# Kernel optimization log

Hardware: AMD Instinct MI355X
Metric: run time of the kernel (lower is better)

The kernel has to match this reference:

```python
import jax, jax.numpy as jnp
import numpy as np

B, L, D = 4, 2048, 512
H, DK, DV = 8, 64, 64


def setup_inputs() -> dict:
    key = jax.random.key(0)
    ks = jax.random.split(key, 12)
    s = 0.02
    return {
        "query": jax.random.normal(ks[0], (B, L, D), jnp.float32),
        "key": jax.random.normal(ks[1], (B, L, D), jnp.float32),
        "value": jax.random.normal(ks[2], (B, L, D), jnp.float32),
        "attention_mask": jax.random.normal(ks[3], (1, 1, L, L), jnp.float32),
        "Wq": jax.random.normal(ks[4], (D, H * DK), jnp.float32) * s,
        "bq": jnp.zeros((H * DK,), jnp.float32),
        "Wk": jax.random.normal(ks[5], (D, H * DK), jnp.float32) * s,
        "bk": jnp.zeros((H * DK,), jnp.float32),
        "Wv": jax.random.normal(ks[6], (D, H * DV), jnp.float32) * s,
        "bv": jnp.zeros((H * DV,), jnp.float32),
        "Wo": jax.random.normal(ks[7], (H * DV, D), jnp.float32) * s,
        "bo": jnp.zeros((D,), jnp.float32),
    }


def reference(query, key, value, attention_mask, Wq, bq, Wk, bk, Wv, bv, Wo, bo):
    sz_b, len_q, _ = query.shape
    len_k = key.shape[1]
    # projections -> [B, L, H, d]
    q = (query @ Wq + bq).reshape(sz_b, len_q, H, DK)
    k = (key @ Wk + bk).reshape(sz_b, len_k, H, DK)
    v = (value @ Wv + bv).reshape(sz_b, len_k, H, DV)
    # permute(2,0,1,3): heads first -> [H, B, L, d]
    q = jnp.transpose(q, (2, 0, 1, 3))
    k = jnp.transpose(k, (2, 0, 1, 3))
    v = jnp.transpose(v, (2, 0, 1, 3))
    scale = 1.0 / jnp.sqrt(jnp.asarray(DK, q.dtype))
    scores = jnp.einsum('hbqd,hbkd->hbqk', q, k) * scale + attention_mask
    attn = jax.nn.softmax(scores, axis=-1)
    x = jnp.einsum('hbqk,hbkd->hbqd', attn, v)  # [H, B, Lq, Dv]
    # faithful to torch: transpose(1,2) -> [H, Lq, B, Dv] then view(B, Lq, H*Dv)
    x = jnp.transpose(x, (0, 2, 1, 3)).reshape(sz_b, len_q, H * DV)
    return x @ Wo + bo
```

## Files before the change

kernel.cpp:

```cpp
#include <hip/hip_runtime.h>

#define SEQ    2048
#define DMODEL 512
#define NHEAD  8
#define HDIM   64
#define BATCH  4
#define NROWS  65536
#define KSPLIT 2

#define LOG2E  1.4426950408889634f
#define QSCALE 0.18033688011112042f

typedef float f32x4  __attribute__((ext_vector_type(4)));
typedef float f32x16 __attribute__((ext_vector_type(16)));
typedef _Float16 h16x8 __attribute__((ext_vector_type(8)));
typedef _Float16 h16x2 __attribute__((ext_vector_type(2)));
typedef unsigned int u32x2 __attribute__((ext_vector_type(2)));

union U4H { uint4 u; h16x8 h; };
union U1H2 { unsigned int u; h16x2 h; };

#define WAITV(N) asm volatile("s_waitcnt vmcnt(" #N ")" ::: "memory")

static __device__ inline h16x2 pkrtz(float a, float b) {
    return __builtin_bit_cast(h16x2, __builtin_amdgcn_cvt_pkrtz(a, b));
}
static __device__ inline unsigned short f2h(float x) {
    _Float16 h = (_Float16)x;
    return __builtin_bit_cast(unsigned short, h);
}
static __device__ inline void async_cp16(const void* g, void* l) {
    __builtin_amdgcn_global_load_lds(
        (const __attribute__((address_space(1))) unsigned int*)g,
        (__attribute__((address_space(3))) unsigned int*)l,
        16, 0, 0);
}

struct PrepArgs {
    const float *Wq, *Wk, *Wv, *Wo;
    unsigned short *WqT, *WkT, *WvT, *WoT;
    const float *mask; unsigned short *mp;
    const float *aq, *ak, *av;
    unsigned short *dq, *dk, *dv;
};

__global__ __launch_bounds__(256) void prepass(PrepArgs a) {
    const int bid = blockIdx.x;
    const int t = threadIdx.x;

    if (bid < 1024) {
        const int z = bid >> 8, y = (bid >> 4) & 15, x = bid & 15;
        const float* S; unsigned short* D;
        switch (z) {
            case 0: S = a.Wq; D = a.WqT; break;
            case 1: S = a.Wk; D = a.WkT; break;
            case 2: S = a.Wv; D = a.WvT; break;
            default: S = a.Wo; D = a.WoT; break;
        }
        __shared__ float T[32][33];
        const int r = t >> 3, c = (t & 7) * 4;
        const int k0 = x * 32, n0 = y * 32;
        float4 v = *(const float4*)&S[(size_t)(k0 + r) * DMODEL + n0 + c];
        T[r][c] = v.x; T[r][c + 1] = v.y; T[r][c + 2] = v.z; T[r][c + 3] = v.w;
        __syncthreads();
        ushort4 o;
        o.x = f2h(T[c + 0][r]); o.y = f2h(T[c + 1][r]);
        o.z = f2h(T[c + 2][r]); o.w = f2h(T[c + 3][r]);
        *(ushort4*)&D[(size_t)(n0 + r) * DMODEL + k0 + c] = o;
    } else if (bid < 1024 + 4096) {
        int i = (bid - 1024) * 256 + t;
        int k = (i * 4) & (SEQ - 1);
        int q = (i * 4) >> 11;
        float4 v = ((const float4*)a.mask)[i];
        int kt = k >> 6, kl = k & 63;
        int mt = kl >> 5, g = (kl >> 3) & 3, hl = (kl >> 2) & 1;
        size_t base = ((size_t)kt * SEQ + q) * 64 + hl * 32 + mt * 16 + g * 4;
        ushort4 o;
        o.x = f2h(__builtin_amdgcn_exp2f(v.x * LOG2E));
        o.y = f2h(__builtin_amdgcn_exp2f(v.y * LOG2E));
        o.z = f2h(__builtin_amdgcn_exp2f(v.z * LOG2E));
        o.w = f2h(__builtin_amdgcn_exp2f(v.w * LOG2E));
        *(ushort4*)&a.mp[base] = o;
    } else {
        int u = bid - 5120;
        int z = u >> 11, blk = u & 2047;
        const float* S; unsigned short* D;
        switch (z) {
            case 0: S = a.aq; D = a.dq; break;
            case 1: S = a.ak; D = a.dk; break;
            default: S = a.av; D = a.dv; break;
        }
        size_t i = ((size_t)blk * 256 + t) * 8;
        float4 x = *(const float4*)&S[i];
        float4 y = *(const float4*)&S[i + 4];
        U1H2 p0, p1, p2, p3;
        p0.h = pkrtz(x.x, x.y); p1.h = pkrtz(x.z, x.w);
        p2.h = pkrtz(y.x, y.y); p3.h = pkrtz(y.z, y.w);
        *(uint4*)&D[i] = make_uint4(p0.u, p1.u, p2.u, p3.u);
    }
}

template <int EPI>
static __device__ inline void gemm_core16(
    const unsigned short* __restrict__ Ab, const unsigned short* __restrict__ Bt,
    const float* __restrict__ bias, void* __restrict__ Cout, float oscale,
    int bm, int bn)
{
    __shared__ __align__(16) unsigned short As[3][128 * 32];
    __shared__ __align__(16) unsigned short Bs[3][128 * 32];

    const int t = threadIdx.x;
    const int lane = t & 63, w = t >> 6;
    const int wm = w >> 1, wn = w & 1;
    const int c = lane & 15, quad = lane >> 4;
    const int srow = lane >> 2;
    const int sck  = (lane & 3) ^ ((lane >> 3) & 3);

    f32x4 acc[4][4] = {};

    const int NT = DMODEL / 32;

    #pragma unroll
    for (int b2 = 0; b2 < 2; b2++) {
        #pragma unroll
        for (int i = 0; i < 2; i++) {
            int row = 32 * w + 16 * i + srow;
            async_cp16(Ab + (size_t)(bm + row) * DMODEL + b2 * 32 + sck * 8,
                       &As[b2][(32 * w + 16 * i) * 32]);
            async_cp16(Bt + (size_t)(bn + row) * DMODEL + b2 * 32 + sck * 8,
                       &Bs[b2][(32 * w + 16 * i) * 32]);
        }
    }
    WAITV(4);
    __builtin_amdgcn_s_barrier();

    const int slot8 = (quad ^ ((c >> 1) & 3)) * 8;

    int cur = 0;
    for (int p = 0; p < NT; p++) {
        if (p + 2 < NT) {
            int nxt = cur + 2; if (nxt >= 3) nxt -= 3;
            int kn = (p + 2) * 32;
            #pragma unroll
            for (int i = 0; i < 2; i++) {
                int row = 32 * w + 16 * i + srow;
                async_cp16(Ab + (size_t)(bm + row) * DMODEL + kn + sck * 8,
                           &As[nxt][(32 * w + 16 * i) * 32]);
                async_cp16(Bt + (size_t)(bn + row) * DMODEL + kn + sck * 8,
                           &Bs[nxt][(32 * w + 16 * i) * 32]);
            }
        }
        U4H af[4], bf[4];
        #pragma unroll
        for (int mt = 0; mt < 4; mt++)
            af[mt].u = *(const uint4*)&As[cur][(wm * 64 + mt * 16 + c) * 32 + slot8];
        #pragma unroll
        for (int nt = 0; nt < 4; nt++)
            bf[nt].u = *(const uint4*)&Bs[cur][(wn * 64 + nt * 16 + c) * 32 + slot8];
        #pragma unroll
        for (int mt = 0; mt < 4; mt++)
            #pragma unroll
            for (int nt = 0; nt < 4; nt++)
                acc[mt][nt] = __builtin_amdgcn_mfma_f32_16x16x32_f16(
                    af[mt].h, bf[nt].h, acc[mt][nt], 0, 0, 0);
        if (p + 1 < NT) {
            if (p + 2 < NT) { WAITV(4); } else { WAITV(0); }
            __builtin_amdgcn_s_barrier();
        }
        cur = cur + 1; if (cur >= 3) cur -= 3;
    }

    if (EPI == 2) {
        #pragma unroll
        for (int nt = 0; nt < 4; nt++) {
            int ng = bn + wn * 64 + nt * 16 + c;
            int h = ng >> 6, dv = ng & 63;
            float bv = bias[ng];
            #pragma unroll
            for (int mt = 0; mt < 4; mt++) {
                int mg0 = bm + wm * 64 + mt * 16 + quad * 4;
                int bb = mg0 >> 11, key0 = mg0 & (SEQ - 1);
                U1H2 lo, hi;
                lo.h = pkrtz(acc[mt][nt][0] + bv, acc[mt][nt][1] + bv);
                hi.h = pkrtz(acc[mt][nt][2] + bv, acc[mt][nt][3] + bv);
                *(uint2*)&((unsigned short*)Cout)[
                    ((size_t)(bb * NHEAD + h) * HDIM + dv) * SEQ + key0] =
                    make_uint2(lo.u, hi.u);
            }
        }
        return;
    }
    #pragma unroll
    for (int nt = 0; nt < 4; nt++) {
        int ng = bn + wn * 64 + nt * 16 + c;
        float bv = bias[ng];
        #pragma unroll
        for (int mt = 0; mt < 4; mt++) {
            #pragma unroll
            for (int r = 0; r < 4; r++) {
                int mg = bm + wm * 64 + mt * 16 + quad * 4 + r;
                float v = (acc[mt][nt][r] + bv) * oscale;
                if (EPI == 1)
                    ((unsigned short*)Cout)[(size_t)mg * DMODEL + ng] = f2h(v);
                else
                    ((float*)Cout)[(size_t)mg * DMODEL + ng] = v;
            }
        }
    }
}

struct QKVArgs {
    const unsigned short *A0, *A1, *A2;
    const unsigned short *W0, *W1, *W2;
    const float *b0, *b1, *b2;
    unsigned short *o0, *o1, *o2;
};

__global__ __launch_bounds__(256) void gemm_qkv(QKVArgs a) {
    if (blockIdx.z == 2)
        gemm_core16<2>(a.A2, a.W2, a.b2, a.o2, 1.0f, blockIdx.y * 128, blockIdx.x * 128);
    else if (blockIdx.z == 1)
        gemm_core16<1>(a.A1, a.W1, a.b1, a.o1, 1.0f, blockIdx.y * 128, blockIdx.x * 128);
    else
        gemm_core16<1>(a.A0, a.W0, a.b0, a.o0, QSCALE, blockIdx.y * 128, blockIdx.x * 128);
}

__global__ __launch_bounds__(256) void gemm_fin(
    const unsigned short* __restrict__ A, const unsigned short* __restrict__ W,
    const float* __restrict__ bias, float* __restrict__ C) {
    gemm_core16<0>(A, W, bias, C, 1.0f, blockIdx.y * 128, blockIdx.x * 128);
}

__global__ __launch_bounds__(256, 3) void attn5(
    const unsigned short* __restrict__ qb, const unsigned short* __restrict__ kb,
    const unsigned short* __restrict__ vT, const unsigned short* __restrict__ emp,
    unsigned short* __restrict__ Xp, float* __restrict__ Lp)
{
    __shared__ __align__(16) unsigned short Ks[3][64 * 64];
    __shared__ __align__(16) unsigned short Vs[3][64 * 64];

    const int t = threadIdx.x;
    const int lane = t & 63, w = t >> 6;
    const int c32 = lane & 31, hl = lane >> 5;
    const int bh = blockIdx.x, b = bh >> 3, head = bh & 7;
    const int q0 = blockIdx.y * 128;
    const int split = blockIdx.z;
    const int qg = q0 + w * 32 + c32;
    const int NT = 1024 / 64;

    const unsigned short* qrow = qb + ((size_t)b * SEQ + qg) * DMODEL + head * HDIM;
    U4H Qf[4];
    #pragma unroll
    for (int s = 0; s < 4; s++)
        Qf[s].u = *(const uint4*)&qrow[s * 16 + hl * 8];

    const unsigned short* kgb = kb + (size_t)b * SEQ * DMODEL + head * HDIM
                              + (size_t)split * 1024 * DMODEL;
    const unsigned short* vgb = vT + (size_t)bh * HDIM * SEQ + split * 1024;

    const int srow = lane >> 3;
    const int sch  = (lane & 7) ^ srow;

    U4H e0, e1, e2, e3;
    {
        const unsigned short* mrow = emp + ((size_t)(split * 16) * SEQ + qg) * 64 + hl * 32;
        e0.u = *(const uint4*)&mrow[0];
        e1.u = *(const uint4*)&mrow[8];
        e2.u = *(const uint4*)&mrow[16];
        e3.u = *(const uint4*)&mrow[24];
    }

    #pragma unroll
    for (int b2 = 0; b2 < 2; b2++) {
        int kq = b2 * 64;
        #pragma unroll
        for (int i = 0; i < 2; i++) {
            int row = w * 16 + i * 8 + srow;
            async_cp16(&kgb[(size_t)(kq + row) * DMODEL + sch * 8],
                       &Ks[b2][(w * 16 + i * 8) * 64]);
            async_cp16(&vgb[(size_t)row * SEQ + kq + sch * 8],
                       &Vs[b2][(w * 16 + i * 8) * 64]);
        }
    }
    WAITV(4);
    __builtin_amdgcn_s_barrier();

    f32x16 O0 = {}, O1 = {};
    float lsum = 0.f;
    const h16x2 one2 = {(_Float16)1.0f, (_Float16)1.0f};

    int cur = 0;
    for (int kt = 0; kt < NT; kt++) {
        U4H f0, f1, f2, f3;
        if (kt + 1 < NT) {
            const unsigned short* mrow =
                emp + ((size_t)(split * 16 + kt + 1) * SEQ + qg) * 64 + hl * 32;
            f0.u = *(const uint4*)&mrow[0];
            f1.u = *(const uint4*)&mrow[8];
            f2.u = *(const uint4*)&mrow[16];
            f3.u = *(const uint4*)&mrow[24];
        }

        if (kt + 2 < NT) {
            int nxt = cur + 2; if (nxt >= 3) nxt -= 3;
            int k0n = (kt + 2) * 64;
            #pragma unroll
            for (int i = 0; i < 2; i++) {
                int row = w * 16 + i * 8 + srow;
                async_cp16(&kgb[(size_t)(k0n + row) * DMODEL + sch * 8],
                           &Ks[nxt][(w * 16 + i * 8) * 64]);
                async_cp16(&vgb[(size_t)row * SEQ + k0n + sch * 8],
                           &Vs[nxt][(w * 16 + i * 8) * 64]);
            }
        }

        const unsigned short* Kp = Ks[cur];
        const unsigned short* Vp = Vs[cur];

        f32x16 S0 = {}, S1 = {};
        __builtin_amdgcn_s_setprio(1);
        #pragma unroll
        for (int s = 0; s < 4; s++) {
            int fc = 2 * s + hl;
            int sl = (fc ^ (c32 & 7)) * 8;
            U4H ka0, ka1;
            ka0.u = *(const uint4*)&Kp[c32 * 64 + sl];
            ka1.u = *(const uint4*)&Kp[(32 + c32) * 64 + sl];
            S0 = __builtin_amdgcn_mfma_f32_32x32x16_f16(ka0.h, Qf[s].h, S0, 0, 0, 0);
            S1 = __builtin_amdgcn_mfma_f32_32x32x16_f16(ka1.h, Qf[s].h, S1, 0, 0, 0);
        }
        __builtin_amdgcn_s_setprio(0);

        unsigned int Pf[4][4];
        #pragma unroll
        for (int mt = 0; mt < 2; mt++) {
            f32x16 S = mt ? S1 : S0;
            h16x8 ea = (mt ? e2 : e0).h;
            h16x8 eb = (mt ? e3 : e1).h;
            unsigned int u[4][2];
            #pragma unroll
            for (int jj = 0; jj < 8; jj++) {
                _Float16 exl = (jj < 4) ? ea[2 * jj]     : eb[2 * jj - 8];
                _Float16 exh = (jj < 4) ? ea[2 * jj + 1] : eb[2 * jj - 7];
                h16x2 ex = {exl, exh};
                h16x2 pk = pkrtz(__builtin_amdgcn_exp2f(S[2 * jj]),
                                 __builtin_amdgcn_exp2f(S[2 * jj + 1]));
                h16x2 pp = pk * ex;
#if __has_builtin(__builtin_amdgcn_fdot2)
                lsum = __builtin_amdgcn_fdot2(pp, one2, lsum, false);
#else
                lsum += (float)pp[0] + (float)pp[1];
#endif
                u[jj >> 1][jj & 1] = __builtin_bit_cast(unsigned int, pp);
            }
#if __has_builtin(__builtin_amdgcn_permlane32_swap)
            u32x2 rA0 = __builtin_amdgcn_permlane32_swap(u[0][0], u[1][0], false, false);
            u32x2 rA1 = __builtin_amdgcn_permlane32_swap(u[0][1], u[1][1], false, false);
            u32x2 rB0 = __builtin_amdgcn_permlane32_swap(u[2][0], u[3][0], false, false);
            u32x2 rB1 = __builtin_amdgcn_permlane32_swap(u[2][1], u[3][1], false, false);
            Pf[2 * mt + 0][0] = rA0[0]; Pf[2 * mt + 0][1] = rA1[0];
            Pf[2 * mt + 0][2] = rA0[1]; Pf[2 * mt + 0][3] = rA1[1];
            Pf[2 * mt + 1][0] = rB0[0]; Pf[2 * mt + 1][1] = rB1[0];
            Pf[2 * mt + 1][2] = rB0[1]; Pf[2 * mt + 1][3] = rB1[1];
#else
            unsigned int sA0 = hl ? u[0][0] : u[1][0];
            unsigned int sA1 = hl ? u[0][1] : u[1][1];
            unsigned int sB0 = hl ? u[2][0] : u[3][0];
            unsigned int sB1 = hl ? u[2][1] : u[3][1];
            unsigned int rA0 = (unsigned)__shfl_xor((int)sA0, 32, 64);
            unsigned int rA1 = (unsigned)__shfl_xor((int)sA1, 32, 64);
            unsigned int rB0 = (unsigned)__shfl_xor((int)sB0, 32, 64);
            unsigned int rB1 = (unsigned)__shfl_xor((int)sB1, 32, 64);
            Pf[2 * mt + 0][0] = hl ? rA0 : u[0][0];
            Pf[2 * mt + 0][1] = hl ? rA1 : u[0][1];
            Pf[2 * mt + 0][2] = hl ? u[1][0] : rA0;
            Pf[2 * mt + 0][3] = hl ? u[1][1] : rA1;
            Pf[2 * mt + 1][0] = hl ? rB0 : u[2][0];
            Pf[2 * mt + 1][1] = hl ? rB1 : u[2][1];
            Pf[2 * mt + 1][2] = hl ? u[3][0] : rB0;
            Pf[2 * mt + 1][3] = hl ? u[3][1] : rB1;
#endif
        }

        __builtin_amdgcn_s_setprio(1);
        #pragma unroll
        for (int s = 0; s < 4; s++) {
            int kc = 2 * s + hl;
            int sl = (kc ^ (c32 & 7)) * 8;
            U4H va0, va1, pu;
            va0.u = *(const uint4*)&Vp[c32 * 64 + sl];
            va1.u = *(const uint4*)&Vp[(32 + c32) * 64 + sl];
            pu.u = make_uint4(Pf[s][0], Pf[s][1], Pf[s][2], Pf[s][3]);
            O0 = __builtin_amdgcn_mfma_f32_32x32x16_f16(va0.h, pu.h, O0, 0, 0, 0);
            O1 = __builtin_amdgcn_mfma_f32_32x32x16_f16(va1.h, pu.h, O1, 0, 0, 0);
        }
        __builtin_amdgcn_s_setprio(0);

        if (kt + 1 < NT) { e0 = f0; e1 = f1; e2 = f2; e3 = f3; }

        if (kt + 1 < NT) {
            if (kt + 2 < NT) { WAITV(8); } else { WAITV(4); }
            __builtin_amdgcn_s_barrier();
        }
        cur = cur + 1; if (cur >= 3) cur -= 3;
    }

    lsum += __shfl_xor(lsum, 32, 64);
    const size_t j = ((size_t)head * SEQ + qg) * BATCH + b;
    unsigned short* xr = Xp + ((size_t)split * NROWS + j) * HDIM;
    #pragma unroll
    for (int mt = 0; mt < 2; mt++) {
        f32x16 Ov = mt ? O1 : O0;
        #pragma unroll
        for (int g = 0; g < 4; g++) {
            U1H2 lo, hi;
            lo.h = pkrtz(Ov[g * 4 + 0], Ov[g * 4 + 1]);
            hi.h = pkrtz(Ov[g * 4 + 2], Ov[g * 4 + 3]);
            uint2 st = make_uint2(lo.u, hi.u);
            *(uint2*)&xr[mt * 32 + 8 * g + 4 * hl] = st;
        }
    }
    if (hl == 0) Lp[split * NROWS + j] = lsum;
}

__global__ __launch_bounds__(256) void combine_attn(
    const unsigned short* __restrict__ Xp, const float* __restrict__ Lp,
    unsigned short* __restrict__ xb)
{
    int i = blockIdx.x * 256 + threadIdx.x;
    int j = i >> 3, dc = (i & 7) * 8;
    U4H a, b;
    a.u = *(const uint4*)&Xp[(size_t)j * HDIM + dc];
    b.u = *(const uint4*)&Xp[((size_t)NROWS + j) * HDIM + dc];
    float inv = 1.0f / (Lp[j] + Lp[NROWS + j]);
    U4H o;
    #pragma unroll
    for (int p = 0; p < 4; p++) {
        float s0 = ((float)a.h[2 * p]     + (float)b.h[2 * p])     * inv;
        float s1 = ((float)a.h[2 * p + 1] + (float)b.h[2 * p + 1]) * inv;
        h16x2 pk = pkrtz(s0, s1);
        o.h[2 * p] = pk[0]; o.h[2 * p + 1] = pk[1];
    }
    *(uint4*)&xb[(size_t)j * HDIM + dc] = o.u;
}

extern "C" void kernel_launch(void* const* d_in, const int* in_sizes, int n_in,
                              void* d_out, int out_size, void* d_ws, size_t ws_size,
                              hipStream_t stream) {
    const float* query = (const float*)d_in[0];
    const float* key_  = (const float*)d_in[1];
    const float* value = (const float*)d_in[2];
    const float* mask  = (const float*)d_in[3];
    const float* Wq = (const float*)d_in[4];
    const float* bq = (const float*)d_in[5];
    const float* Wk = (const float*)d_in[6];
    const float* bk = (const float*)d_in[7];
    const float* Wv = (const float*)d_in[8];
    const float* bv = (const float*)d_in[9];
    const float* Wo = (const float*)d_in[10];
    const float* bo = (const float*)d_in[11];
    float* out = (float*)d_out;

    const size_t NP = (size_t)BATCH * SEQ * DMODEL;
    unsigned short* ws   = (unsigned short*)d_ws;
    unsigned short* qb16 = ws;
    unsigned short* kb16 = qb16 + NP;
    unsigned short* vT16 = kb16 + NP;
    unsigned short* xb16 = vT16 + NP;
    unsigned short* em16 = xb16 + NP;
    unsigned short* Xp16 = em16 + (size_t)SEQ * SEQ;
    unsigned short* WqT  = Xp16 + (size_t)KSPLIT * NROWS * HDIM;
    unsigned short* WkT  = WqT + DMODEL * DMODEL;
    unsigned short* WvT  = WkT + DMODEL * DMODEL;
    unsigned short* WoT  = WvT + DMODEL * DMODEL;
    float* Lp = (float*)(WoT + DMODEL * DMODEL);

    unsigned short* q16 = xb16;
    unsigned short* k16 = Xp16;
    unsigned short* v16 = Xp16 + NP;

    PrepArgs pa;
    pa.Wq = Wq; pa.Wk = Wk; pa.Wv = Wv; pa.Wo = Wo;
    pa.WqT = WqT; pa.WkT = WkT; pa.WvT = WvT; pa.WoT = WoT;
    pa.mask = mask; pa.mp = em16;
    pa.aq = query; pa.ak = key_; pa.av = value;
    pa.dq = q16; pa.dk = k16; pa.dv = v16;
    prepass<<<dim3(1024 + 4096 + 6144), 256, 0, stream>>>(pa);

    QKVArgs qa;
    qa.A0 = q16;  qa.A1 = k16;  qa.A2 = v16;
    qa.W0 = WqT;  qa.W1 = WkT;  qa.W2 = WvT;
    qa.b0 = bq;   qa.b1 = bk;   qa.b2 = bv;
    qa.o0 = qb16; qa.o1 = kb16; qa.o2 = vT16;
    gemm_qkv<<<dim3(DMODEL / 128, BATCH * SEQ / 128, 3), 256, 0, stream>>>(qa);

    attn5<<<dim3(BATCH * NHEAD, SEQ / 128, KSPLIT), 256, 0, stream>>>(
        qb16, kb16, vT16, em16, Xp16, Lp);

    combine_attn<<<dim3(NROWS * 8 / 256), 256, 0, stream>>>(Xp16, Lp, xb16);

    gemm_fin<<<dim3(DMODEL / 128, BATCH * SEQ / 128), 256, 0, stream>>>(
        xb16, WoT, bo, out);
}
```

Baseline: 231.7 us.

## Fuse split-K attention combine into output GEMM and enlarge attention blocks

Removes the separate combine_attn kernel. The output projection GEMM now loads both partial attention outputs and their softmax sums, normalises them, and writes the combined fp16 tile straight into shared memory as its A operand. This saves a kernel launch and a full round trip of the combined activations through global memory. Separately, the attention kernel now runs 512-thread blocks covering 256 query rows, so each K/V tile in shared memory serves twice as many queries and each wave issues fewer async copies. The cost is larger blocks and a new launch bound of (512, 6) that may constrain registers.

```diff
diff --git a/kernel.cpp b/kernel.cpp
--- a/kernel.cpp
+++ b/kernel.cpp
@@ -200,10 +200,7 @@
             for (int r = 0; r < 4; r++) {
                 int mg = bm + wm * 64 + mt * 16 + quad * 4 + r;
                 float v = (acc[mt][nt][r] + bv) * oscale;
-                if (EPI == 1)
-                    ((unsigned short*)Cout)[(size_t)mg * DMODEL + ng] = f2h(v);
-                else
-                    ((float*)Cout)[(size_t)mg * DMODEL + ng] = v;
+                ((unsigned short*)Cout)[(size_t)mg * DMODEL + ng] = f2h(v);
             }
         }
     }
@@ -226,12 +223,108 @@
 }
 
 __global__ __launch_bounds__(256) void gemm_fin(
-    const unsigned short* __restrict__ A, const unsigned short* __restrict__ W,
-    const float* __restrict__ bias, float* __restrict__ C) {
-    gemm_core16<0>(A, W, bias, C, 1.0f, blockIdx.y * 128, blockIdx.x * 128);
-}
-
-__global__ __launch_bounds__(256, 3) void attn5(
+    const unsigned short* __restrict__ Xp, const float* __restrict__ Lp,
+    const unsigned short* __restrict__ Wt, const float* __restrict__ bias,
+    float* __restrict__ C)
+{
+    __shared__ __align__(16) unsigned short As[2][128 * 32];
+    __shared__ __align__(16) unsigned short Bs[2][128 * 32];
+
+    const int t = threadIdx.x;
+    const int lane = t & 63, w = t >> 6;
+    const int wm = w >> 1, wn = w & 1;
+    const int c = lane & 15, quad = lane >> 4;
+    const int bm = (int)blockIdx.y * 128, bn = (int)blockIdx.x * 128;
+    const int srow = lane >> 2;
+    const int sck  = (lane & 3) ^ ((lane >> 3) & 3);
+    const int arow = t >> 2, afc = t & 3;
+
+    f32x4 acc[4][4] = {};
+
+    U4H a0, b0, a1, b1; float i0, i1;
+    auto loadA = [&](int k0) {
+        int jc = k0 >> 6, dv = (k0 & 32) + afc * 8;
+        int j0 = (bm + arow) * 8 + jc;
+        int j1 = (bm + 64 + arow) * 8 + jc;
+        a0.u = *(const uint4*)&Xp[(size_t)j0 * HDIM + dv];
+        b0.u = *(const uint4*)&Xp[((size_t)NROWS + j0) * HDIM + dv];
+        a1.u = *(const uint4*)&Xp[(size_t)j1 * HDIM + dv];
+        b1.u = *(const uint4*)&Xp[((size_t)NROWS + j1) * HDIM + dv];
+        i0 = 1.0f / (Lp[j0] + Lp[NROWS + j0]);
+        i1 = 1.0f / (Lp[j1] + Lp[NROWS + j1]);
+    };
+    auto writeA = [&](int buf, U4H a, U4H b, float inv, int row) {
+        U4H o;
+        #pragma unroll
+        for (int e = 0; e < 4; e++) {
+            float s0 = ((float)a.h[2 * e]     + (float)b.h[2 * e])     * inv;
+            float s1 = ((float)a.h[2 * e + 1] + (float)b.h[2 * e + 1]) * inv;
+            h16x2 pk = pkrtz(s0, s1);
+            o.h[2 * e] = pk[0]; o.h[2 * e + 1] = pk[1];
+        }
+        *(uint4*)&As[buf][row * 32 + ((afc ^ ((row >> 1) & 3))) * 8] = o.u;
+    };
+
+    loadA(0);
+    #pragma unroll
+    for (int i = 0; i < 2; i++) {
+        int row = 32 * w + 16 * i + srow;
+        async_cp16(Wt + (size_t)(bn + row) * DMODEL + sck * 8,
+                   &Bs[0][(32 * w + 16 * i) * 32]);
+    }
+    writeA(0, a0, b0, i0, arow);
+    writeA(0, a1, b1, i1, 64 + arow);
+    __syncthreads();
+
+    const int slot8 = (quad ^ ((c >> 1) & 3)) * 8;
+
+    for (int k0 = 0; k0 < DMODEL; k0 += 32) {
+        const int cur = (k0 >> 5) & 1;
+        if (k0 + 32 < DMODEL) {
+            loadA(k0 + 32);
+            #pragma unroll
+            for (int i = 0; i < 2; i++) {
+                int row = 32 * w + 16 * i + srow;
+                async_cp16(Wt + (size_t)(bn + row) * DMODEL + k0 + 32 + sck * 8,
+                           &Bs[cur ^ 1][(32 * w + 16 * i) * 32]);
+            }
+        }
+        U4H af[4], bf[4];
+        #pragma unroll
+        for (int mt = 0; mt < 4; mt++)
+            af[mt].u = *(const uint4*)&As[cur][(wm * 64 + mt * 16 + c) * 32 + slot8];
+        #pragma unroll
+        for (int nt = 0; nt < 4; nt++)
+            bf[nt].u = *(const uint4*)&Bs[cur][(wn * 64 + nt * 16 + c) * 32 + slot8];
+        #pragma unroll
+        for (int mt = 0; mt < 4; mt++)
+            #pragma unroll
+            for (int nt = 0; nt < 4; nt++)
+                acc[mt][nt] = __builtin_amdgcn_mfma_f32_16x16x32_f16(
+                    af[mt].h, bf[nt].h, acc[mt][nt], 0, 0, 0);
+        if (k0 + 32 < DMODEL) {
+            writeA(cur ^ 1, a0, b0, i0, arow);
+            writeA(cur ^ 1, a1, b1, i1, 64 + arow);
+        }
+        __syncthreads();
+    }
+
+    #pragma unroll
+    for (int nt = 0; nt < 4; nt++) {
+        int ng = bn + wn * 64 + nt * 16 + c;
+        float bv = bias[ng];
+        #pragma unroll
+        for (int mt = 0; mt < 4; mt++) {
+            #pragma unroll
+            for (int r = 0; r < 4; r++) {
+                int mg = bm + wm * 64 + mt * 16 + quad * 4 + r;
+                C[(size_t)mg * DMODEL + ng] = acc[mt][nt][r] + bv;
+            }
+        }
+    }
+}
+
+__global__ __launch_bounds__(512, 6) void attn5(
     const unsigned short* __restrict__ qb, const unsigned short* __restrict__ kb,
     const unsigned short* __restrict__ vT, const unsigned short* __restrict__ emp,
     unsigned short* __restrict__ Xp, float* __restrict__ Lp)
@@ -243,7 +336,7 @@
     const int lane = t & 63, w = t >> 6;
     const int c32 = lane & 31, hl = lane >> 5;
     const int bh = blockIdx.x, b = bh >> 3, head = bh & 7;
-    const int q0 = blockIdx.y * 128;
+    const int q0 = blockIdx.y * 256;
     const int split = blockIdx.z;
     const int qg = q0 + w * 32 + c32;
     const int NT = 1024 / 64;
@@ -273,16 +366,13 @@
     #pragma unroll
     for (int b2 = 0; b2 < 2; b2++) {
         int kq = b2 * 64;
-        #pragma unroll
-        for (int i = 0; i < 2; i++) {
-            int row = w * 16 + i * 8 + srow;
-            async_cp16(&kgb[(size_t)(kq + row) * DMODEL + sch * 8],
-                       &Ks[b2][(w * 16 + i * 8) * 64]);
-            async_cp16(&vgb[(size_t)row * SEQ + kq + sch * 8],
-                       &Vs[b2][(w * 16 + i * 8) * 64]);
-        }
-    }
-    WAITV(4);
+        int row = w * 8 + srow;
+        async_cp16(&kgb[(size_t)(kq + row) * DMODEL + sch * 8],
+                   &Ks[b2][(w * 8) * 64]);
+        async_cp16(&vgb[(size_t)row * SEQ + kq + sch * 8],
+                   &Vs[b2][(w * 8) * 64]);
+    }
+    WAITV(2);
     __builtin_amdgcn_s_barrier();
 
     f32x16 O0 = {}, O1 = {};
@@ -304,14 +394,11 @@
         if (kt + 2 < NT) {
             int nxt = cur + 2; if (nxt >= 3) nxt -= 3;
             int k0n = (kt + 2) * 64;
-            #pragma unroll
-            for (int i = 0; i < 2; i++) {
-                int row = w * 16 + i * 8 + srow;
-                async_cp16(&kgb[(size_t)(k0n + row) * DMODEL + sch * 8],
-                           &Ks[nxt][(w * 16 + i * 8) * 64]);
-                async_cp16(&vgb[(size_t)row * SEQ + k0n + sch * 8],
-                           &Vs[nxt][(w * 16 + i * 8) * 64]);
-            }
+            int row = w * 8 + srow;
+            async_cp16(&kgb[(size_t)(k0n + row) * DMODEL + sch * 8],
+                       &Ks[nxt][(w * 8) * 64]);
+            async_cp16(&vgb[(size_t)row * SEQ + k0n + sch * 8],
+                       &Vs[nxt][(w * 8) * 64]);
         }
 
         const unsigned short* Kp = Ks[cur];
@@ -399,7 +486,7 @@
         if (kt + 1 < NT) { e0 = f0; e1 = f1; e2 = f2; e3 = f3; }
 
         if (kt + 1 < NT) {
-            if (kt + 2 < NT) { WAITV(8); } else { WAITV(4); }
+            if (kt + 2 < NT) { WAITV(2); } else { WAITV(4); }
             __builtin_amdgcn_s_barrier();
         }
         cur = cur + 1; if (cur >= 3) cur -= 3;
@@ -421,27 +508,6 @@
         }
     }
     if (hl == 0) Lp[split * NROWS + j] = lsum;
-}
-
-__global__ __launch_bounds__(256) void combine_attn(
-    const unsigned short* __restrict__ Xp, const float* __restrict__ Lp,
-    unsigned short* __restrict__ xb)
-{
-    int i = blockIdx.x * 256 + threadIdx.x;
-    int j = i >> 3, dc = (i & 7) * 8;
-    U4H a, b;
-    a.u = *(const uint4*)&Xp[(size_t)j * HDIM + dc];
-    b.u = *(const uint4*)&Xp[((size_t)NROWS + j) * HDIM + dc];
-    float inv = 1.0f / (Lp[j] + Lp[NROWS + j]);
-    U4H o;
-    #pragma unroll
-    for (int p = 0; p < 4; p++) {
-        float s0 = ((float)a.h[2 * p]     + (float)b.h[2 * p])     * inv;
-        float s1 = ((float)a.h[2 * p + 1] + (float)b.h[2 * p + 1]) * inv;
-        h16x2 pk = pkrtz(s0, s1);
-        o.h[2 * p] = pk[0]; o.h[2 * p + 1] = pk[1];
-    }
-    *(uint4*)&xb[(size_t)j * HDIM + dc] = o.u;
 }
 
 extern "C" void kernel_launch(void* const* d_in, const int* in_sizes, int n_in,
@@ -494,11 +560,9 @@
     qa.o0 = qb16; qa.o1 = kb16; qa.o2 = vT16;
     gemm_qkv<<<dim3(DMODEL / 128, BATCH * SEQ / 128, 3), 256, 0, stream>>>(qa);
 
-    attn5<<<dim3(BATCH * NHEAD, SEQ / 128, KSPLIT), 256, 0, stream>>>(
+    attn5<<<dim3(BATCH * NHEAD, SEQ / 256, KSPLIT), 512, 0, stream>>>(
         qb16, kb16, vT16, em16, Xp16, Lp);
 
-    combine_attn<<<dim3(NROWS * 8 / 256), 256, 0, stream>>>(Xp16, Lp, xb16);
-
     gemm_fin<<<dim3(DMODEL / 128, BATCH * SEQ / 128), 256, 0, stream>>>(
-        xb16, WoT, bo, out);
-}
+        Xp16, Lp, WoT, bo, out);
+}
```

New measurement: 478.1 us. +106.4%, slower.

## Process two heads per 512-thread attention block with double-buffered K/V tiles

Applied to the files above, without the earlier changes.

The attention kernel now runs blocks of 512 threads (8 waves), where each group of 4 waves handles a different head of the same batch and query tile. The grid halves in the head dimension. The 3-stage K/V ring buffer with 2-tile prefetch is replaced by a 2-stage double buffer with 1-tile prefetch, and every iteration waits for all outstanding loads (vmcnt 0). This spreads each block's loads over more waves and drops the occupancy hint of 3 blocks. In exchange it exposes more global-load latency through the shallower pipeline and full waits.

```diff
diff --git a/kernel.cpp b/kernel.cpp
--- a/kernel.cpp
+++ b/kernel.cpp
@@ -231,21 +231,25 @@
     gemm_core16<0>(A, W, bias, C, 1.0f, blockIdx.y * 128, blockIdx.x * 128);
 }
 
-__global__ __launch_bounds__(256, 3) void attn5(
+__global__ __launch_bounds__(512) void attn5(
     const unsigned short* __restrict__ qb, const unsigned short* __restrict__ kb,
     const unsigned short* __restrict__ vT, const unsigned short* __restrict__ emp,
     unsigned short* __restrict__ Xp, float* __restrict__ Lp)
 {
-    __shared__ __align__(16) unsigned short Ks[3][64 * 64];
-    __shared__ __align__(16) unsigned short Vs[3][64 * 64];
+    __shared__ __align__(16) unsigned short Ks[2][2][64 * 64];
+    __shared__ __align__(16) unsigned short Vs[2][2][64 * 64];
 
     const int t = threadIdx.x;
     const int lane = t & 63, w = t >> 6;
+    const int g = w >> 2;
     const int c32 = lane & 31, hl = lane >> 5;
-    const int bh = blockIdx.x, b = bh >> 3, head = bh & 7;
+    const int pr = blockIdx.x;
+    const int b = pr >> 2;
+    const int headA = (2 * pr) & 7;
+    const int head = headA + g;
     const int q0 = blockIdx.y * 128;
     const int split = blockIdx.z;
-    const int qg = q0 + w * 32 + c32;
+    const int qg = q0 + (w & 3) * 32 + c32;
     const int NT = 1024 / 64;
 
     const unsigned short* qrow = qb + ((size_t)b * SEQ + qg) * DMODEL + head * HDIM;
@@ -254,12 +258,15 @@
     for (int s = 0; s < 4; s++)
         Qf[s].u = *(const uint4*)&qrow[s * 16 + hl * 8];
 
-    const unsigned short* kgb = kb + (size_t)b * SEQ * DMODEL + head * HDIM
-                              + (size_t)split * 1024 * DMODEL;
-    const unsigned short* vgb = vT + (size_t)bh * HDIM * SEQ + split * 1024;
+    const unsigned short* kgbA = kb + (size_t)b * SEQ * DMODEL + headA * HDIM
+                               + (size_t)split * 1024 * DMODEL;
+    const unsigned short* kgbB = kgbA + HDIM;
+    const unsigned short* vgbA = vT + (size_t)(2 * pr) * HDIM * SEQ + split * 1024;
+    const unsigned short* vgbB = vgbA + (size_t)HDIM * SEQ;
 
     const int srow = lane >> 3;
     const int sch  = (lane & 7) ^ srow;
+    const int sr = w * 8 + srow;
 
     U4H e0, e1, e2, e3;
     {
@@ -270,19 +277,11 @@
         e3.u = *(const uint4*)&mrow[24];
     }
 
-    #pragma unroll
-    for (int b2 = 0; b2 < 2; b2++) {
-        int kq = b2 * 64;
-        #pragma unroll
-        for (int i = 0; i < 2; i++) {
-            int row = w * 16 + i * 8 + srow;
-            async_cp16(&kgb[(size_t)(kq + row) * DMODEL + sch * 8],
-                       &Ks[b2][(w * 16 + i * 8) * 64]);
-            async_cp16(&vgb[(size_t)row * SEQ + kq + sch * 8],
-                       &Vs[b2][(w * 16 + i * 8) * 64]);
-        }
-    }
-    WAITV(4);
+    async_cp16(&kgbA[(size_t)sr * DMODEL + sch * 8], &Ks[0][0][(w * 8) * 64]);
+    async_cp16(&vgbA[(size_t)sr * SEQ + sch * 8],    &Vs[0][0][(w * 8) * 64]);
+    async_cp16(&kgbB[(size_t)sr * DMODEL + sch * 8], &Ks[0][1][(w * 8) * 64]);
+    async_cp16(&vgbB[(size_t)sr * SEQ + sch * 8],    &Vs[0][1][(w * 8) * 64]);
+    WAITV(0);
     __builtin_amdgcn_s_barrier();
 
     f32x16 O0 = {}, O1 = {};
@@ -301,21 +300,20 @@
             f3.u = *(const uint4*)&mrow[24];
         }
 
-        if (kt + 2 < NT) {
-            int nxt = cur + 2; if (nxt >= 3) nxt -= 3;
-            int k0n = (kt + 2) * 64;
-            #pragma unroll
-            for (int i = 0; i < 2; i++) {
-                int row = w * 16 + i * 8 + srow;
-                async_cp16(&kgb[(size_t)(k0n + row) * DMODEL + sch * 8],
-                           &Ks[nxt][(w * 16 + i * 8) * 64]);
-                async_cp16(&vgb[(size_t)row * SEQ + k0n + sch * 8],
-                           &Vs[nxt][(w * 16 + i * 8) * 64]);
-            }
-        }
-
-        const unsigned short* Kp = Ks[cur];
-        const unsigned short* Vp = Vs[cur];
+        if (kt + 1 < NT) {
+            int k0n = (kt + 1) * 64;
+            async_cp16(&kgbA[(size_t)(k0n + sr) * DMODEL + sch * 8],
+                       &Ks[cur ^ 1][0][(w * 8) * 64]);
+            async_cp16(&vgbA[(size_t)sr * SEQ + k0n + sch * 8],
+                       &Vs[cur ^ 1][0][(w * 8) * 64]);
+            async_cp16(&kgbB[(size_t)(k0n + sr) * DMODEL + sch * 8],
+                       &Ks[cur ^ 1][1][(w * 8) * 64]);
+            async_cp16(&vgbB[(size_t)sr * SEQ + k0n + sch * 8],
+                       &Vs[cur ^ 1][1][(w * 8) * 64]);
+        }
+
+        const unsigned short* Kp = &Ks[cur][g][0];
+        const unsigned short* Vp = &Vs[cur][g][0];
 
         f32x16 S0 = {}, S1 = {};
         __builtin_amdgcn_s_setprio(1);
@@ -396,13 +394,12 @@
         }
         __builtin_amdgcn_s_setprio(0);
 
-        if (kt + 1 < NT) { e0 = f0; e1 = f1; e2 = f2; e3 = f3; }
-
         if (kt + 1 < NT) {
-            if (kt + 2 < NT) { WAITV(8); } else { WAITV(4); }
+            WAITV(0);
             __builtin_amdgcn_s_barrier();
-        }
-        cur = cur + 1; if (cur >= 3) cur -= 3;
+            e0 = f0; e1 = f1; e2 = f2; e3 = f3;
+        }
+        cur ^= 1;
     }
 
     lsum += __shfl_xor(lsum, 32, 64);
@@ -412,12 +409,12 @@
     for (int mt = 0; mt < 2; mt++) {
         f32x16 Ov = mt ? O1 : O0;
         #pragma unroll
-        for (int g = 0; g < 4; g++) {
+        for (int gi = 0; gi < 4; gi++) {
             U1H2 lo, hi;
-            lo.h = pkrtz(Ov[g * 4 + 0], Ov[g * 4 + 1]);
-            hi.h = pkrtz(Ov[g * 4 + 2], Ov[g * 4 + 3]);
+            lo.h = pkrtz(Ov[gi * 4 + 0], Ov[gi * 4 + 1]);
+            hi.h = pkrtz(Ov[gi * 4 + 2], Ov[gi * 4 + 3]);
             uint2 st = make_uint2(lo.u, hi.u);
-            *(uint2*)&xr[mt * 32 + 8 * g + 4 * hl] = st;
+            *(uint2*)&xr[mt * 32 + 8 * gi + 4 * hl] = st;
         }
     }
     if (hl == 0) Lp[split * NROWS + j] = lsum;
@@ -494,7 +491,7 @@
     qa.o0 = qb16; qa.o1 = kb16; qa.o2 = vT16;
     gemm_qkv<<<dim3(DMODEL / 128, BATCH * SEQ / 128, 3), 256, 0, stream>>>(qa);
 
-    attn5<<<dim3(BATCH * NHEAD, SEQ / 128, KSPLIT), 256, 0, stream>>>(
+    attn5<<<dim3(BATCH * NHEAD / 2, SEQ / 128, KSPLIT), 512, 0, stream>>>(
         qb16, kb16, vT16, em16, Xp16, Lp);
 
     combine_attn<<<dim3(NROWS * 8 / 256), 256, 0, stream>>>(Xp16, Lp, xb16);
```

Measured after the change: 251.6 us. 8.6% more time.

## Halve attention KV tile to 32 keys, shrink LDS and registers

Applied to the files above, without the earlier changes.

The attention kernel now walks keys in 32-wide tiles instead of 64, halving the K/V shared-memory ring buffers and the score and mask registers per iteration. The LDS swizzle is rewritten to suit the new 32-column V layout, the mask prefetch indexing is adjusted, and the 3-blocks-per-SM launch bound hint is removed. The aim is to cut register and LDS pressure so more waves can run concurrently. In exchange the loop runs twice as many iterations, with twice as many barriers and waits and less MFMA work between them to hide latency.

```diff
diff --git a/kernel.cpp b/kernel.cpp
--- a/kernel.cpp
+++ b/kernel.cpp
@@ -231,13 +231,13 @@
     gemm_core16<0>(A, W, bias, C, 1.0f, blockIdx.y * 128, blockIdx.x * 128);
 }
 
-__global__ __launch_bounds__(256, 3) void attn5(
+__global__ __launch_bounds__(256) void attn5(
     const unsigned short* __restrict__ qb, const unsigned short* __restrict__ kb,
     const unsigned short* __restrict__ vT, const unsigned short* __restrict__ emp,
     unsigned short* __restrict__ Xp, float* __restrict__ Lp)
 {
-    __shared__ __align__(16) unsigned short Ks[3][64 * 64];
-    __shared__ __align__(16) unsigned short Vs[3][64 * 64];
+    __shared__ __align__(16) unsigned short Ks[3][32 * 64];
+    __shared__ __align__(16) unsigned short Vs[3][64 * 32];
 
     const int t = threadIdx.x;
     const int lane = t & 63, w = t >> 6;
@@ -246,7 +246,7 @@
     const int q0 = blockIdx.y * 128;
     const int split = blockIdx.z;
     const int qg = q0 + w * 32 + c32;
-    const int NT = 1024 / 64;
+    const int NT = 1024 / 32;
 
     const unsigned short* qrow = qb + ((size_t)b * SEQ + qg) * DMODEL + head * HDIM;
     U4H Qf[4];
@@ -258,85 +258,77 @@
                               + (size_t)split * 1024 * DMODEL;
     const unsigned short* vgb = vT + (size_t)bh * HDIM * SEQ + split * 1024;
 
-    const int srow = lane >> 3;
-    const int sch  = (lane & 7) ^ srow;
-
-    U4H e0, e1, e2, e3;
+    const int krow = w * 8 + (lane >> 3);
+    const int kch  = (lane & 7) ^ ((krow + (krow >> 3)) & 7);
+    const int vrow = w * 16 + (lane >> 2);
+    const int vch  = (lane & 3) ^ ((vrow + (vrow >> 2)) & 3);
+
+    U4H e0, e1;
     {
-        const unsigned short* mrow = emp + ((size_t)(split * 16) * SEQ + qg) * 64 + hl * 32;
+        const int g32 = split * 32;
+        const unsigned short* mrow = emp + ((size_t)(g32 >> 1) * SEQ + qg) * 64
+                                   + hl * 32 + (g32 & 1) * 16;
         e0.u = *(const uint4*)&mrow[0];
         e1.u = *(const uint4*)&mrow[8];
-        e2.u = *(const uint4*)&mrow[16];
-        e3.u = *(const uint4*)&mrow[24];
     }
 
     #pragma unroll
     for (int b2 = 0; b2 < 2; b2++) {
-        int kq = b2 * 64;
-        #pragma unroll
-        for (int i = 0; i < 2; i++) {
-            int row = w * 16 + i * 8 + srow;
-            async_cp16(&kgb[(size_t)(kq + row) * DMODEL + sch * 8],
-                       &Ks[b2][(w * 16 + i * 8) * 64]);
-            async_cp16(&vgb[(size_t)row * SEQ + kq + sch * 8],
-                       &Vs[b2][(w * 16 + i * 8) * 64]);
-        }
-    }
-    WAITV(4);
+        int kq = b2 * 32;
+        async_cp16(&kgb[(size_t)(kq + krow) * DMODEL + kch * 8],
+                   &Ks[b2][(w * 8) * 64]);
+        async_cp16(&vgb[(size_t)vrow * SEQ + kq + vch * 8],
+                   &Vs[b2][(w * 16) * 32]);
+    }
+    WAITV(2);
     __builtin_amdgcn_s_barrier();
 
     f32x16 O0 = {}, O1 = {};
     float lsum = 0.f;
     const h16x2 one2 = {(_Float16)1.0f, (_Float16)1.0f};
 
+    const int skq = (c32 + (c32 >> 3)) & 7;
+    const int svq = (c32 + (c32 >> 2)) & 3;
+
     int cur = 0;
     for (int kt = 0; kt < NT; kt++) {
-        U4H f0, f1, f2, f3;
+        U4H f0, f1;
         if (kt + 1 < NT) {
-            const unsigned short* mrow =
-                emp + ((size_t)(split * 16 + kt + 1) * SEQ + qg) * 64 + hl * 32;
+            const int g32 = split * 32 + kt + 1;
+            const unsigned short* mrow = emp + ((size_t)(g32 >> 1) * SEQ + qg) * 64
+                                       + hl * 32 + (g32 & 1) * 16;
             f0.u = *(const uint4*)&mrow[0];
             f1.u = *(const uint4*)&mrow[8];
-            f2.u = *(const uint4*)&mrow[16];
-            f3.u = *(const uint4*)&mrow[24];
         }
 
         if (kt + 2 < NT) {
             int nxt = cur + 2; if (nxt >= 3) nxt -= 3;
-            int k0n = (kt + 2) * 64;
-            #pragma unroll
-            for (int i = 0; i < 2; i++) {
-                int row = w * 16 + i * 8 + srow;
-                async_cp16(&kgb[(size_t)(k0n + row) * DMODEL + sch * 8],
-                           &Ks[nxt][(w * 16 + i * 8) * 64]);
-                async_cp16(&vgb[(size_t)row * SEQ + k0n + sch * 8],
-                           &Vs[nxt][(w * 16 + i * 8) * 64]);
-            }
+            int k0n = (kt + 2) * 32;
+            async_cp16(&kgb[(size_t)(k0n + krow) * DMODEL + kch * 8],
+                       &Ks[nxt][(w * 8) * 64]);
+            async_cp16(&vgb[(size_t)vrow * SEQ + k0n + vch * 8],
+                       &Vs[nxt][(w * 16) * 32]);
         }
 
         const unsigned short* Kp = Ks[cur];
         const unsigned short* Vp = Vs[cur];
 
-        f32x16 S0 = {}, S1 = {};
+        f32x16 S = {};
         __builtin_amdgcn_s_setprio(1);
         #pragma unroll
         for (int s = 0; s < 4; s++) {
             int fc = 2 * s + hl;
-            int sl = (fc ^ (c32 & 7)) * 8;
-            U4H ka0, ka1;
-            ka0.u = *(const uint4*)&Kp[c32 * 64 + sl];
-            ka1.u = *(const uint4*)&Kp[(32 + c32) * 64 + sl];
-            S0 = __builtin_amdgcn_mfma_f32_32x32x16_f16(ka0.h, Qf[s].h, S0, 0, 0, 0);
-            S1 = __builtin_amdgcn_mfma_f32_32x32x16_f16(ka1.h, Qf[s].h, S1, 0, 0, 0);
+            int sl = (fc ^ skq) * 8;
+            U4H ka;
+            ka.u = *(const uint4*)&Kp[c32 * 64 + sl];
+            S = __builtin_amdgcn_mfma_f32_32x32x16_f16(ka.h, Qf[s].h, S, 0, 0, 0);
         }
         __builtin_amdgcn_s_setprio(0);
 
-        unsigned int Pf[4][4];
-        #pragma unroll
-        for (int mt = 0; mt < 2; mt++) {
-            f32x16 S = mt ? S1 : S0;
-            h16x8 ea = (mt ? e2 : e0).h;
-            h16x8 eb = (mt ? e3 : e1).h;
+        unsigned int Pf[2][4];
+        {
+            h16x8 ea = e0.h;
+            h16x8 eb = e1.h;
             unsigned int u[4][2];
             #pragma unroll
             for (int jj = 0; jj < 8; jj++) {
@@ -358,10 +350,8 @@
             u32x2 rA1 = __builtin_amdgcn_permlane32_swap(u[0][1], u[1][1], false, false);
             u32x2 rB0 = __builtin_amdgcn_permlane32_swap(u[2][0], u[3][0], false, false);
             u32x2 rB1 = __builtin_amdgcn_permlane32_swap(u[2][1], u[3][1], false, false);
-            Pf[2 * mt + 0][0] = rA0[0]; Pf[2 * mt + 0][1] = rA1[0];
-            Pf[2 * mt + 0][2] = rA0[1]; Pf[2 * mt + 0][3] = rA1[1];
-            Pf[2 * mt + 1][0] = rB0[0]; Pf[2 * mt + 1][1] = rB1[0];
-            Pf[2 * mt + 1][2] = rB0[1]; Pf[2 * mt + 1][3] = rB1[1];
+            Pf[0][0] = rA0[0]; Pf[0][1] = rA1[0]; Pf[0][2] = rA0[1]; Pf[0][3] = rA1[1];
+            Pf[1][0] = rB0[0]; Pf[1][1] = rB1[0]; Pf[1][2] = rB0[1]; Pf[1][3] = rB1[1];
 #else
             unsigned int sA0 = hl ? u[0][0] : u[1][0];
             unsigned int sA1 = hl ? u[0][1] : u[1][1];
@@ -371,35 +361,35 @@
             unsigned int rA1 = (unsigned)__shfl_xor((int)sA1, 32, 64);
             unsigned int rB0 = (unsigned)__shfl_xor((int)sB0, 32, 64);
             unsigned int rB1 = (unsigned)__shfl_xor((int)sB1, 32, 64);
-            Pf[2 * mt + 0][0] = hl ? rA0 : u[0][0];
-            Pf[2 * mt + 0][1] = hl ? rA1 : u[0][1];
-            Pf[2 * mt + 0][2] = hl ? u[1][0] : rA0;
-            Pf[2 * mt + 0][3] = hl ? u[1][1] : rA1;
-            Pf[2 * mt + 1][0] = hl ? rB0 : u[2][0];
-            Pf[2 * mt + 1][1] = hl ? rB1 : u[2][1];
-            Pf[2 * mt + 1][2] = hl ? u[3][0] : rB0;
-            Pf[2 * mt + 1][3] = hl ? u[3][1] : rB1;
+            Pf[0][0] = hl ? rA0 : u[0][0];
+            Pf[0][1] = hl ? rA1 : u[0][1];
+            Pf[0][2] = hl ? u[1][0] : rA0;
+            Pf[0][3] = hl ? u[1][1] : rA1;
+            Pf[1][0] = hl ? rB0 : u[2][0];
+            Pf[1][1] = hl ? rB1 : u[2][1];
+            Pf[1][2] = hl ? u[3][0] : rB0;
+            Pf[1][3] = hl ? u[3][1] : rB1;
 #endif
         }
 
         __builtin_amdgcn_s_setprio(1);
         #pragma unroll
-        for (int s = 0; s < 4; s++) {
+        for (int s = 0; s < 2; s++) {
             int kc = 2 * s + hl;
-            int sl = (kc ^ (c32 & 7)) * 8;
+            int sl = (kc ^ svq) * 8;
             U4H va0, va1, pu;
-            va0.u = *(const uint4*)&Vp[c32 * 64 + sl];
-            va1.u = *(const uint4*)&Vp[(32 + c32) * 64 + sl];
+            va0.u = *(const uint4*)&Vp[c32 * 32 + sl];
+            va1.u = *(const uint4*)&Vp[(32 + c32) * 32 + sl];
             pu.u = make_uint4(Pf[s][0], Pf[s][1], Pf[s][2], Pf[s][3]);
             O0 = __builtin_amdgcn_mfma_f32_32x32x16_f16(va0.h, pu.h, O0, 0, 0, 0);
             O1 = __builtin_amdgcn_mfma_f32_32x32x16_f16(va1.h, pu.h, O1, 0, 0, 0);
         }
         __builtin_amdgcn_s_setprio(0);
 
-        if (kt + 1 < NT) { e0 = f0; e1 = f1; e2 = f2; e3 = f3; }
+        if (kt + 1 < NT) { e0 = f0; e1 = f1; }
 
         if (kt + 1 < NT) {
-            if (kt + 2 < NT) { WAITV(8); } else { WAITV(4); }
+            if (kt + 2 < NT) { WAITV(4); } else { WAITV(2); }
             __builtin_amdgcn_s_barrier();
         }
         cur = cur + 1; if (cur >= 3) cur -= 3;
```

New measurement: 233.3 us. Within noise of the previous version (+0.7%).
